# Performance work log

Hardware: AMD Instinct MI355X
Metric: run time of the kernel (lower is better)

## Reference

```python
import jax, jax.numpy as jnp
import numpy as np

B, L, E, H = 4, 1024, 1024, 16
D = E // H  # head_dim = 64
K = 3       # conv kernel size
PROB = 0.9  # Bernoulli keep probability


def setup_inputs() -> dict:
    key = jax.random.key(0)
    ks = jax.random.split(key, 8)
    query = jax.random.normal(ks[0], (B, L, E), dtype=jnp.float32)
    keys = jax.random.normal(ks[1], (B, L, E), dtype=jnp.float32)
    values = jax.random.normal(ks[2], (B, L, E), dtype=jnp.float32)
    padding_mask = jax.random.randint(ks[3], (B, L), 0, 2, dtype=jnp.int32)
    causal_mask = jax.random.randint(ks[4], (B, L), 0, 2, dtype=jnp.int32)
    bern_mask = jax.random.bernoulli(ks[5], PROB, (B, H, L)).astype(jnp.int32)
    # learned params: grouped conv (one in/out channel per head) and value linear
    conv_w = jax.random.normal(ks[6], (H, 1, K, K), dtype=jnp.float32) * 0.1
    conv_b = jnp.zeros((H,), dtype=jnp.float32)
    Wv = jax.random.normal(ks[7], (D, D), dtype=jnp.float32) / np.sqrt(D)
    return {"query": query, "keys": keys, "values": values,
            "padding_mask": padding_mask, "causal_mask": causal_mask,
            "bern_mask": bern_mask, "conv_w": conv_w, "conv_b": conv_b, "Wv": Wv}


def _split_heads(x):  # [b, l, (h d)] -> [b, h, l, d]
    b, l, _ = x.shape
    return x.reshape(b, l, H, D).transpose(0, 2, 1, 3)


def reference(query, keys, values, padding_mask, causal_mask, bern_mask, conv_w, conv_b, Wv):
    # queries: grouped conv2d over [b, h=channels, l, d], shape-preserving
    q = _split_heads(query)
    q = jax.lax.conv_general_dilated(
        q, conv_w, window_strides=(1, 1), padding=((1, 1), (1, 1)),
        dimension_numbers=("NCHW", "OIHW", "NCHW"), feature_group_count=H)
    q = q + conv_b[None, :, None, None]
    # keys: Bernoulli-masked fill with -inf, softmax over the SEQ dim (dim=-2)
    k = _split_heads(keys)
    k = jnp.where(bern_mask[..., None].astype(bool), k, -jnp.inf)
    k = jax.nn.softmax(k, axis=-2)
    # values: per-head linear (torch Linear: x @ W^T)
    v = jnp.einsum("bhld,ed->bhle", _split_heads(values), Wv)
    # attention
    energy = jnp.einsum("bhqd,bhkd->bhqk", q, k)
    mask = (padding_mask.astype(bool) & causal_mask.astype(bool))  # [b, k]
    energy = jnp.where(mask[:, None, None, :], jnp.float32(-1e20), energy)
    attn = jax.nn.softmax(energy / jnp.sqrt(jnp.float32(E)), axis=-1)
    out = jnp.einsum("bhqk,bhkd->bhqd", attn, v)
    return out.transpose(0, 2, 1, 3).reshape(query.shape[0], query.shape[1], E)
```

## Files before the change

kernel.cpp:

```cpp
#include <hip/hip_runtime.h>
#include <hip/hip_bf16.h>
#include <math.h>

#define BB 4
#define LL 1024
#define EE 1024
#define HH 16
#define DD 64
#define VROWS 80
#define NCH 8
#define CHROWS 128
#define K2C 0.04508422002777998f

typedef __attribute__((ext_vector_type(8))) short short8;
typedef __attribute__((ext_vector_type(4))) float f32x4;
typedef __attribute__((ext_vector_type(4))) int int4v;

static __device__ __forceinline__ unsigned short bfbits(float x) {
    __hip_bfloat16 h = __float2bfloat16(x);
    return *(unsigned short*)&h;
}
static __device__ __forceinline__ float bf2f(unsigned short u) {
    unsigned int x = (unsigned int)u << 16;
    return *(float*)&x;
}

#define CVTPK(dst, lo_, hi_) \
    asm("v_cvt_pk_bf16_f32 %0, %1, %2" : "=v"(dst) : "v"(lo_), "v"(hi_))

__global__ __launch_bounds__(256) void prep_kernel(
    const float* __restrict__ query,
    const float* __restrict__ conv_w,
    const float* __restrict__ conv_b,
    const float* __restrict__ values,
    const float* __restrict__ Wv,
    const float* __restrict__ keys,
    const int* __restrict__ bern,
    const int* __restrict__ pad,
    const int* __restrict__ cau,
    __hip_bfloat16* __restrict__ qcb,
    __hip_bfloat16* __restrict__ vt,
    __hip_bfloat16* __restrict__ ksb,
    float* __restrict__ psum) {
    __shared__ __align__(16) char SM[34304];
    int tid = threadIdx.x;
    int bid = blockIdx.x;

    if (bid < 4096) {
        int d = tid & 63;
        int lr = tid >> 6;
        int l0 = (bid & (LL / 4 - 1)) << 2;
        int bh = bid >> 8;
        int h = bh & (HH - 1);
        int b = bh >> 4;
        int l = l0 + lr;

        const float* w = conv_w + h * 9;
        float acc = conv_b[h];
        const float* qin = query + ((size_t)b * LL) * EE + h * DD;
        #pragma unroll
        for (int i = 0; i < 3; ++i) {
            int li = l + i - 1;
            if (li < 0 || li >= LL) continue;
            #pragma unroll
            for (int j = 0; j < 3; ++j) {
                int dj = d + j - 1;
                if (dj < 0 || dj >= DD) continue;
                acc += w[i * 3 + j] * qin[(size_t)li * EE + dj];
            }
        }
        qcb[((size_t)bh * LL + l) * DD + d] = __float2bfloat16(acc * K2C);
    } else if (bid < 5120) {
        float (*WvS)[65] = (float(*)[65])SM;
        float (*vs)[68]  = (float(*)[68])(SM + 16640);
        float* mS = (float*)(SM + 34048);
        int tile = bid - 4096;
        int lt = tile & 15;
        int bh = tile >> 4;
        int h = bh & (HH - 1);
        int b = bh >> 4;
        int l0 = lt * 64;

        if (tid < 64) {
            int l = l0 + tid;
            mS[tid] = ((pad[b * LL + l] != 0) & (cau[b * LL + l] != 0)) ? 0.f : 1.f;
        }
        for (int idx = tid; idx < 64 * 64; idx += 256)
            WvS[idx >> 6][idx & 63] = Wv[idx];
        const float* vin = values + ((size_t)b * LL + l0) * EE + h * DD;
        for (int idx = tid; idx < 1024; idx += 256) {
            int r = idx >> 4;
            int c4 = (idx & 15) << 2;
            *(float4*)&vs[r][c4] = *(const float4*)&vin[(size_t)r * EE + c4];
        }
        __syncthreads();

        int d = tid & 63;
        int r0 = (tid >> 6) * 16;
        float acc[16];
        #pragma unroll
        for (int r = 0; r < 16; ++r) acc[r] = 0.f;
        for (int k = 0; k < 64; ++k) {
            float wv = WvS[d][k];
            #pragma unroll
            for (int r = 0; r < 16; ++r) acc[r] += vs[r0 + r][k] * wv;
        }
        #pragma unroll
        for (int r = 0; r < 16; ++r) acc[r] *= mS[r0 + r];
        union { unsigned short us[16]; uint2 u2[4]; } pk;
        #pragma unroll
        for (int r = 0; r < 16; ++r) pk.us[r] = bfbits(acc[r]);
        int a = tid >> 6;
        int C32 = (a >> 1) << 5;
        int h4 = a & 1;
        __hip_bfloat16* vo = vt + ((size_t)bh * VROWS + d) * LL + l0 + C32 + 4 * h4;
        #pragma unroll
        for (int g2 = 0; g2 < 4; ++g2)
            *(uint2*)&vo[8 * g2] = pk.u2[g2];

        if (tid < 64) {
            int aa = tid >> 4, g2 = (tid >> 2) & 3, m = tid & 3;
            int dst = l0 + 32 * (aa >> 1) + 4 * (aa & 1) + 8 * g2 + m;
            vt[((size_t)bh * VROWS + 64) * LL + dst] = __float2bfloat16(mS[tid]);
        }
        for (int idx = tid; idx < 15 * 64; idx += 256) {
            int rr = idx >> 6, l = idx & 63;
            vt[((size_t)bh * VROWS + 65 + rr) * LL + l0 + l] = __float2bfloat16(0.f);
        }
    } else {
        float (*ss)[64] = (float(*)[64])SM;
        int blk = bid - 5120;
        int d = tid & 63;
        int seg = tid >> 6;
        int ch = blk & (NCH - 1);
        int bh = blk >> 3;
        int h = bh & (HH - 1);
        int b = bh >> 4;
        int r0 = ch * CHROWS + seg * 32;

        const float* kin = keys + ((size_t)b * LL + r0) * EE + h * DD + d;
        const int* bm = bern + (size_t)bh * LL + r0;
        __hip_bfloat16* kout = ksb + ((size_t)bh * LL + r0) * DD + d;

        float s = 0.f;
        #pragma unroll
        for (int i = 0; i < 32; ++i) {
            float ek = bm[i] ? __expf(kin[(size_t)i * EE]) : 0.f;
            s += ek;
            kout[(size_t)i * DD] = __float2bfloat16(ek);
        }
        ss[seg][d] = s;
        __syncthreads();
        if (seg == 0) {
            float S = (ss[0][d] + ss[1][d]) + (ss[2][d] + ss[3][d]);
            psum[(size_t)blk * 64 + d] = S;
        }
    }
}

__global__ __launch_bounds__(256) void invs_kernel(
    const float* __restrict__ psum,
    float* __restrict__ invS) {
    int idx = blockIdx.x * 256 + threadIdx.x;
    int bh = idx >> 6;
    int d = idx & 63;
    const float* p = psum + (size_t)bh * NCH * 64 + d;
    float S = 0.f;
    #pragma unroll
    for (int c = 0; c < NCH; ++c) S += p[c * 64];
    invS[idx] = 1.f / S;
}

__global__ __launch_bounds__(256) void attn_mfma_kernel(
    const __hip_bfloat16* __restrict__ qcb,
    const __hip_bfloat16* __restrict__ ksb,
    const __hip_bfloat16* __restrict__ vtb,
    const float* __restrict__ invS,
    float* __restrict__ out) {
    __shared__ __align__(16) short KsS[2][4096];
    __shared__ __align__(16) short VtS[2][5120];

    int tid = threadIdx.x;
    int lane = tid & 63;
    int w = tid >> 6;
    int q15 = lane & 15;
    int g = (lane >> 4) & 3;

    int bid = blockIdx.x;
    int swz = (bid & 7) * 128 + (bid >> 3);
    int bh = swz >> 4;
    int qb = swz & 15;
    int b = bh >> 4;
    int h = bh & 15;
    int q0w = qb * 64 + w * 16;

    int srow = tid >> 3;
    int sch = tid & 7;
    int ssw = (sch ^ (srow & 7)) << 3;
    const short* kg = (const short*)ksb + (size_t)bh * LL * DD + (size_t)srow * DD + ssw;
    const short* vg = (const short*)vtb + (size_t)bh * VROWS * LL + (size_t)srow * LL + ssw;
    const short* vgx = (const short*)vtb + (size_t)bh * VROWS * LL + (size_t)(64 + srow) * LL + ssw;

    short8 Qf0, Qf1;
    {
        const short* qrow = (const short*)qcb + ((size_t)bh * LL + q0w + q15) * DD + 8 * g;
        short8 r0 = *(const short8*)(qrow);
        short8 r1 = *(const short8*)(qrow + 32);
        const float* isb = invS + (size_t)bh * 64 + 8 * g;
        #pragma unroll
        for (int j = 0; j < 8; ++j) {
            Qf0[j] = (short)bfbits(bf2f((unsigned short)r0[j]) * isb[j]);
            Qf1[j] = (short)bfbits(bf2f((unsigned short)r1[j]) * isb[32 + j]);
        }
    }

    #pragma unroll
    for (int it = 0; it < 2; ++it) {
        __builtin_amdgcn_global_load_lds(
            (const __attribute__((address_space(1))) void*)(kg + (size_t)(it * 32) * DD),
            (__attribute__((address_space(3))) void*)&KsS[0][(it * 4 + w) * 512], 16, 0, 0);
        __builtin_amdgcn_global_load_lds(
            (const __attribute__((address_space(1))) void*)(vg + (size_t)it * 32 * LL),
            (__attribute__((address_space(3))) void*)&VtS[0][(it * 4 + w) * 512], 16, 0, 0);
    }
    if (w < 2) {
        __builtin_amdgcn_global_load_lds(
            (const __attribute__((address_space(1))) void*)(vgx),
            (__attribute__((address_space(3))) void*)&VtS[0][4096 + w * 512], 16, 0, 0);
    }

    f32x4 O[4], O5;
    #pragma unroll
    for (int u = 0; u < 4; ++u) O[u] = (f32x4){0.f, 0.f, 0.f, 0.f};
    O5 = (f32x4){0.f, 0.f, 0.f, 0.f};

    for (int kt = 0; kt < 16; ++kt) {
        __syncthreads();

        if (kt < 15) {
            int nb = (kt + 1) & 1;
            int k0n = (kt + 1) * 64;
            #pragma unroll
            for (int it = 0; it < 2; ++it) {
                __builtin_amdgcn_global_load_lds(
                    (const __attribute__((address_space(1))) void*)(kg + (size_t)(k0n + it * 32) * DD),
                    (__attribute__((address_space(3))) void*)&KsS[nb][(it * 4 + w) * 512], 16, 0, 0);
                __builtin_amdgcn_global_load_lds(
                    (const __attribute__((address_space(1))) void*)(vg + k0n + (size_t)it * 32 * LL),
                    (__attribute__((address_space(3))) void*)&VtS[nb][(it * 4 + w) * 512], 16, 0, 0);
            }
            if (w < 2) {
                __builtin_amdgcn_global_load_lds(
                    (const __attribute__((address_space(1))) void*)(vgx + k0n),
                    (__attribute__((address_space(3))) void*)&VtS[nb][4096 + w * 512], 16, 0, 0);
            }
        }

        int cb = kt & 1;
        const short* Kb = KsS[cb];
        const short* Vb = VtS[cb];
        int sw = q15 & 7;
        int off0 = (g ^ sw) << 3;
        int off1 = ((g + 4) ^ sw) << 3;

        f32x4 S[4];
        __builtin_amdgcn_s_setprio(1);
        #pragma unroll
        for (int t = 0; t < 4; ++t) {
            short8 kf0 = *(const short8*)&Kb[(16 * t + q15) * 64 + off0];
            short8 kf1 = *(const short8*)&Kb[(16 * t + q15) * 64 + off1];
            f32x4 z = (f32x4){0.f, 0.f, 0.f, 0.f};
            z = __builtin_amdgcn_mfma_f32_16x16x32_bf16(kf0, Qf0, z, 0, 0, 0);
            S[t] = __builtin_amdgcn_mfma_f32_16x16x32_bf16(kf1, Qf1, z, 0, 0, 0);
        }
        __builtin_amdgcn_s_setprio(0);

        short8 vfa[5], vfb[5];
        #pragma unroll
        for (int u = 0; u < 5; ++u) {
            vfa[u] = *(const short8*)&Vb[(16 * u + q15) * 64 + off0];
            vfb[u] = *(const short8*)&Vb[(16 * u + q15) * 64 + off1];
        }

        float pv[4][4];
        #pragma unroll
        for (int t = 0; t < 4; ++t)
            #pragma unroll
            for (int r = 0; r < 4; ++r)
                pv[t][r] = exp2f(S[t][r]);

        int4v pa0, pa1;
        {
            int d0, d1, d2, d3;
            CVTPK(d0, pv[0][0], pv[0][1]);
            CVTPK(d1, pv[0][2], pv[0][3]);
            CVTPK(d2, pv[1][0], pv[1][1]);
            CVTPK(d3, pv[1][2], pv[1][3]);
            pa0 = (int4v){d0, d1, d2, d3};
            CVTPK(d0, pv[2][0], pv[2][1]);
            CVTPK(d1, pv[2][2], pv[2][3]);
            CVTPK(d2, pv[3][0], pv[3][1]);
            CVTPK(d3, pv[3][2], pv[3][3]);
            pa1 = (int4v){d0, d1, d2, d3};
        }
        union PW { int4v i4; short8 s8; } pw0, pw1;
        pw0.i4 = pa0;
        pw1.i4 = pa1;

        __builtin_amdgcn_s_setprio(1);
        #pragma unroll
        for (int u = 0; u < 4; ++u) {
            O[u] = __builtin_amdgcn_mfma_f32_16x16x32_bf16(vfa[u], pw0.s8, O[u], 0, 0, 0);
            O[u] = __builtin_amdgcn_mfma_f32_16x16x32_bf16(vfb[u], pw1.s8, O[u], 0, 0, 0);
        }
        O5 = __builtin_amdgcn_mfma_f32_16x16x32_bf16(vfa[4], pw0.s8, O5, 0, 0, 0);
        O5 = __builtin_amdgcn_mfma_f32_16x16x32_bf16(vfb[4], pw1.s8, O5, 0, 0, 0);
        __builtin_amdgcn_s_setprio(0);
    }

    float ls = __shfl(O5[0], q15, 64);
    float invl = 1.f / ls;

    float* gout = out + ((size_t)b * LL + q0w + q15) * EE + h * DD + 4 * g;
    #pragma unroll
    for (int u = 0; u < 4; ++u) {
        float4 vv = { O[u][0] * invl, O[u][1] * invl, O[u][2] * invl, O[u][3] * invl };
        *(float4*)&gout[16 * u] = vv;
    }
}

extern "C" void kernel_launch(void* const* d_in, const int* in_sizes, int n_in,
                              void* d_out, int out_size, void* d_ws, size_t ws_size,
                              hipStream_t stream) {
    const float* query = (const float*)d_in[0];
    const float* keys  = (const float*)d_in[1];
    const float* values = (const float*)d_in[2];
    const int* pad  = (const int*)d_in[3];
    const int* cau  = (const int*)d_in[4];
    const int* bern = (const int*)d_in[5];
    const float* conv_w = (const float*)d_in[6];
    const float* conv_b = (const float*)d_in[7];
    const float* Wv = (const float*)d_in[8];
    float* outp = (float*)d_out;

    const size_t per = (size_t)BB * HH * LL * DD;
    const size_t vper = (size_t)BB * HH * VROWS * LL;
    __hip_bfloat16* qcb = (__hip_bfloat16*)d_ws;
    __hip_bfloat16* ksb = qcb + per;
    __hip_bfloat16* vtb = ksb + per;
    float* psum = (float*)(vtb + vper);
    float* invS = psum + (size_t)BB * HH * NCH * 64;

    prep_kernel<<<5632, 256, 0, stream>>>(query, conv_w, conv_b, values, Wv,
                                          keys, bern, pad, cau,
                                          qcb, vtb, ksb, psum);
    invs_kernel<<<16, 256, 0, stream>>>(psum, invS);
    attn_mfma_kernel<<<BB * HH * 16, 256, 0, stream>>>(qcb, ksb, vtb, invS, outp);
}
```

Baseline: 76.17 us.

## Restructure prep kernel: tiled conv via LDS, interleaved block roles, pre-transposed Wv

The query conv now loads a 34-row halo tile into shared memory and has each thread compute 8 rows, replacing scattered per-element global reads. Block roles (conv, value projection, key exp) are interleaved by blockIdx mod 4 so heterogeneous work is mixed across CUs, and key chunks are halved so the grid is balanced at 4096 blocks. A tiny new kernel transposes Wv once so value blocks read it straight from global/L2 instead of staging it in LDS, which cuts shared memory per block and may raise occupancy. The cost is an extra kernel launch and more partial sums in the reduction.

```diff
diff --git a/kernel.cpp b/kernel.cpp
--- a/kernel.cpp
+++ b/kernel.cpp
@@ -8,8 +8,8 @@
 #define HH 16
 #define DD 64
 #define VROWS 80
-#define NCH 8
-#define CHROWS 128
+#define NCH2 16
+#define CH2ROWS 64
 #define K2C 0.04508422002777998f
 
 typedef __attribute__((ext_vector_type(8))) short short8;
@@ -27,13 +27,20 @@
 
 #define CVTPK(dst, lo_, hi_) \
     asm("v_cvt_pk_bf16_f32 %0, %1, %2" : "=v"(dst) : "v"(lo_), "v"(hi_))
+
+__global__ __launch_bounds__(256) void wvt_kernel(
+    const float* __restrict__ Wv, float* __restrict__ WvT) {
+    int idx = blockIdx.x * 256 + threadIdx.x;
+    int k = idx >> 6, e = idx & 63;
+    WvT[idx] = Wv[e * 64 + k];
+}
 
 __global__ __launch_bounds__(256) void prep_kernel(
     const float* __restrict__ query,
     const float* __restrict__ conv_w,
     const float* __restrict__ conv_b,
     const float* __restrict__ values,
-    const float* __restrict__ Wv,
+    const float* __restrict__ WvT,
     const float* __restrict__ keys,
     const int* __restrict__ bern,
     const int* __restrict__ pad,
@@ -42,39 +49,62 @@
     __hip_bfloat16* __restrict__ vt,
     __hip_bfloat16* __restrict__ ksb,
     float* __restrict__ psum) {
-    __shared__ __align__(16) char SM[34304];
+    __shared__ __align__(16) char SM[17664];
     int tid = threadIdx.x;
     int bid = blockIdx.x;
-
-    if (bid < 4096) {
-        int d = tid & 63;
-        int lr = tid >> 6;
-        int l0 = (bid & (LL / 4 - 1)) << 2;
-        int bh = bid >> 8;
+    int type = bid & 3;
+
+    if (type < 2) {
+        float (*qs)[64] = (float(*)[64])SM;
+        int tile = ((bid >> 2) << 1) | (bid & 1);
+        int lt = tile & 31;
+        int bh = tile >> 5;
         int h = bh & (HH - 1);
         int b = bh >> 4;
-        int l = l0 + lr;
-
+        int l0 = lt * 32;
+
+        const float* qin = query + ((size_t)b * LL) * EE + h * DD;
+        for (int idx = tid; idx < 34 * 16; idx += 256) {
+            int row = idx >> 4;
+            int c4 = (idx & 15) << 2;
+            int gl = l0 + row - 1;
+            float4 v = (gl >= 0 && gl < LL)
+                ? *(const float4*)&qin[(size_t)gl * EE + c4]
+                : (float4){0.f, 0.f, 0.f, 0.f};
+            *(float4*)&qs[row][c4] = v;
+        }
+        __syncthreads();
+
+        int d = tid & 63;
+        int a = tid >> 6;
         const float* w = conv_w + h * 9;
-        float acc = conv_b[h];
-        const float* qin = query + ((size_t)b * LL) * EE + h * DD;
-        #pragma unroll
-        for (int i = 0; i < 3; ++i) {
-            int li = l + i - 1;
-            if (li < 0 || li >= LL) continue;
+        float w00 = w[0], w01 = w[1], w02 = w[2];
+        float w10 = w[3], w11 = w[4], w12 = w[5];
+        float w20 = w[6], w21 = w[7], w22 = w[8];
+        float bias = conv_b[h];
+        __hip_bfloat16* qo = qcb + ((size_t)bh * LL + l0 + a * 8) * DD + d;
+        #pragma unroll
+        for (int r = 0; r < 8; ++r) {
+            int l = a * 8 + r;
+            float acc = bias;
             #pragma unroll
-            for (int j = 0; j < 3; ++j) {
-                int dj = d + j - 1;
-                if (dj < 0 || dj >= DD) continue;
-                acc += w[i * 3 + j] * qin[(size_t)li * EE + dj];
+            for (int i = 0; i < 3; ++i) {
+                float mid = qs[l + i][d];
+                float lft = (d > 0) ? qs[l + i][d - 1] : 0.f;
+                float rgt = (d < 63) ? qs[l + i][d + 1] : 0.f;
+                float wi0 = (i == 0) ? w00 : (i == 1) ? w10 : w20;
+                float wi1 = (i == 0) ? w01 : (i == 1) ? w11 : w21;
+                float wi2 = (i == 0) ? w02 : (i == 1) ? w12 : w22;
+                acc = __builtin_fmaf(wi0, lft, acc);
+                acc = __builtin_fmaf(wi1, mid, acc);
+                acc = __builtin_fmaf(wi2, rgt, acc);
             }
-        }
-        qcb[((size_t)bh * LL + l) * DD + d] = __float2bfloat16(acc * K2C);
-    } else if (bid < 5120) {
-        float (*WvS)[65] = (float(*)[65])SM;
-        float (*vs)[68]  = (float(*)[68])(SM + 16640);
-        float* mS = (float*)(SM + 34048);
-        int tile = bid - 4096;
+            qo[(size_t)r * DD] = __float2bfloat16(acc * K2C);
+        }
+    } else if (type == 2) {
+        float (*vs)[68] = (float(*)[68])SM;
+        float* mS = (float*)(SM + 17408);
+        int tile = bid >> 2;
         int lt = tile & 15;
         int bh = tile >> 4;
         int h = bh & (HH - 1);
@@ -85,8 +115,6 @@
             int l = l0 + tid;
             mS[tid] = ((pad[b * LL + l] != 0) & (cau[b * LL + l] != 0)) ? 0.f : 1.f;
         }
-        for (int idx = tid; idx < 64 * 64; idx += 256)
-            WvS[idx >> 6][idx & 63] = Wv[idx];
         const float* vin = values + ((size_t)b * LL + l0) * EE + h * DD;
         for (int idx = tid; idx < 1024; idx += 256) {
             int r = idx >> 4;
@@ -101,7 +129,7 @@
         #pragma unroll
         for (int r = 0; r < 16; ++r) acc[r] = 0.f;
         for (int k = 0; k < 64; ++k) {
-            float wv = WvS[d][k];
+            float wv = WvT[k * 64 + d];
             #pragma unroll
             for (int r = 0; r < 16; ++r) acc[r] += vs[r0 + r][k] * wv;
         }
@@ -129,14 +157,14 @@
         }
     } else {
         float (*ss)[64] = (float(*)[64])SM;
-        int blk = bid - 5120;
+        int tile = bid >> 2;
+        int ch = tile & (NCH2 - 1);
+        int bh = tile >> 4;
+        int h = bh & (HH - 1);
+        int b = bh >> 4;
         int d = tid & 63;
         int seg = tid >> 6;
-        int ch = blk & (NCH - 1);
-        int bh = blk >> 3;
-        int h = bh & (HH - 1);
-        int b = bh >> 4;
-        int r0 = ch * CHROWS + seg * 32;
+        int r0 = ch * CH2ROWS + seg * 16;
 
         const float* kin = keys + ((size_t)b * LL + r0) * EE + h * DD + d;
         const int* bm = bern + (size_t)bh * LL + r0;
@@ -144,7 +172,7 @@
 
         float s = 0.f;
         #pragma unroll
-        for (int i = 0; i < 32; ++i) {
+        for (int i = 0; i < 16; ++i) {
             float ek = bm[i] ? __expf(kin[(size_t)i * EE]) : 0.f;
             s += ek;
             kout[(size_t)i * DD] = __float2bfloat16(ek);
@@ -153,7 +181,7 @@
         __syncthreads();
         if (seg == 0) {
             float S = (ss[0][d] + ss[1][d]) + (ss[2][d] + ss[3][d]);
-            psum[(size_t)blk * 64 + d] = S;
+            psum[(size_t)tile * 64 + d] = S;
         }
     }
 }
@@ -164,10 +192,10 @@
     int idx = blockIdx.x * 256 + threadIdx.x;
     int bh = idx >> 6;
     int d = idx & 63;
-    const float* p = psum + (size_t)bh * NCH * 64 + d;
+    const float* p = psum + (size_t)bh * NCH2 * 64 + d;
     float S = 0.f;
     #pragma unroll
-    for (int c = 0; c < NCH; ++c) S += p[c * 64];
+    for (int c = 0; c < NCH2; ++c) S += p[c * 64];
     invS[idx] = 1.f / S;
 }
 
@@ -349,9 +377,11 @@
     __hip_bfloat16* ksb = qcb + per;
     __hip_bfloat16* vtb = ksb + per;
     float* psum = (float*)(vtb + vper);
-    float* invS = psum + (size_t)BB * HH * NCH * 64;
-
-    prep_kernel<<<5632, 256, 0, stream>>>(query, conv_w, conv_b, values, Wv,
+    float* invS = psum + (size_t)BB * HH * NCH2 * 64;
+    float* WvT  = invS + (size_t)BB * HH * 64;
+
+    wvt_kernel<<<16, 256, 0, stream>>>(Wv, WvT);
+    prep_kernel<<<4096, 256, 0, stream>>>(query, conv_w, conv_b, values, WvT,
                                           keys, bern, pad, cau,
                                           qcb, vtb, ksb, psum);
     invs_kernel<<<16, 256, 0, stream>>>(psum, invS);
```

Result: slower. 99.84 us (+31.1%).
